# Performance work log

Measured on AMD Instinct MI355X. Metric: run time of the kernel, lower is better.

Reference implementation:

```python
import jax, jax.numpy as jnp
import numpy as np

N_NODES = 50000
N_EDGES = 800000
HID = 64
N_LAYERS = 4
POS_DIM = 3
PARAM_SCALE = 0.1
POS_HEAD_SCALE = 0.001  # xavier gain=0.001 on final pos Linear


def setup_inputs() -> dict:
    key = jax.random.key(0)
    ks = jax.random.split(key, 12)
    L, H = N_LAYERS, HID
    s = PARAM_SCALE
    return {
        "x": jax.random.normal(ks[0], (N_NODES, HID), jnp.float32),
        "pos": jax.random.normal(ks[1], (N_NODES, POS_DIM), jnp.float32),
        "edge_index": jax.random.randint(ks[2], (2, N_EDGES), 0, N_NODES, jnp.int32),
        # edge MLP: Linear(2H+1 -> H), SiLU, Linear(H -> H), SiLU
        "We1": jax.random.normal(ks[3], (L, 2 * H + 1, H), jnp.float32) * s,
        "be1": jnp.zeros((L, H), jnp.float32),
        "We2": jax.random.normal(ks[4], (L, H, H), jnp.float32) * s,
        "be2": jnp.zeros((L, H), jnp.float32),
        # node MLP: Linear(2H -> H), SiLU, Linear(H -> H)
        "Wn1": jax.random.normal(ks[5], (L, 2 * H, H), jnp.float32) * s,
        "bn1": jnp.zeros((L, H), jnp.float32),
        "Wn2": jax.random.normal(ks[6], (L, H, H), jnp.float32) * s,
        "bn2": jnp.zeros((L, H), jnp.float32),
        # pos MLP: Linear(H -> H), SiLU, Linear(H -> 1) (tiny init)
        "Wp1": jax.random.normal(ks[7], (L, H, H), jnp.float32) * s,
        "bp1": jnp.zeros((L, H), jnp.float32),
        "Wp2": jax.random.normal(ks[8], (L, H, 1), jnp.float32) * POS_HEAD_SCALE,
        "bp2": jnp.zeros((L, 1), jnp.float32),
        # logit(pos_scale=0.5) == 0
        "pos_scale_logit": jnp.zeros((1,), jnp.float32),
    }


def reference(x, pos, edge_index, We1, be1, We2, be2, Wn1, bn1, Wn2, bn2,
              Wp1, bp1, Wp2, bp2, pos_scale_logit):
    POS_CLAMP = 500.0
    POS_UPDATE_CLAMP = 5.0
    src, dst = edge_index[0], edge_index[1]  # messages flow j=src -> i=dst
    n = x.shape[0]
    L = We1.shape[0]

    # pos is NOT fed back between layers in the torch forward, so edge
    # geometry is constant across layers.
    rel = pos[dst] - pos[src]                     # [E, P]
    d2 = jnp.sum(rel * rel, axis=-1, keepdims=True)  # [E, 1]
    deg = jnp.maximum(
        jax.ops.segment_sum(jnp.ones(src.shape, x.dtype), dst, num_segments=n),
        1.0)[:, None]                             # [N, 1]

    pos_new = pos
    for l in range(L):
        # edge MLP on gathered node pairs
        m = jnp.concatenate([x[dst], x[src], d2], axis=-1)  # [E, 2H+1]
        m = jax.nn.silu(m @ We1[l] + be1[l])
        m = jax.nn.silu(m @ We2[l] + be2[l])                # [E, H]
        # scatter-aggregate messages to target nodes
        agg = jax.ops.segment_sum(m, dst, num_segments=n)   # [N, H]
        # node update MLP
        h = jax.nn.silu(jnp.concatenate([x, agg], axis=-1) @ Wn1[l] + bn1[l])
        x = h @ Wn2[l] + bn2[l]
        # position update: mean over incoming edges of rel * phi_pos(m)
        c = jax.nn.silu(m @ Wp1[l] + bp1[l]) @ Wp2[l] + bp2[l]  # [E, 1]
        pos_new = pos + jax.ops.segment_sum(rel * c, dst, num_segments=n) / deg

    upd = (pos_new - pos) * jax.nn.sigmoid(pos_scale_logit[0])
    upd = jnp.clip(upd, -POS_UPDATE_CLAMP, POS_UPDATE_CLAMP)
    pos_out = jnp.clip(pos + upd, -POS_CLAMP, POS_CLAMP)
    return x, pos_out
```

## Files before the change

kernel.cpp:

```cpp
#include <hip/hip_runtime.h>

#define NN 50000
#define NE 800000
#define NTILES 12500
#define TPB 10

typedef __attribute__((ext_vector_type(8))) short short8;
typedef __attribute__((ext_vector_type(4))) float f32x4;

__device__ __forceinline__ float silu_f(float v) {
    return v / (1.0f + __expf(-v));
}
__device__ __forceinline__ unsigned short f2bf(float f) {
    unsigned u = __float_as_uint(f);
    u += 0x7fffu + ((u >> 16) & 1u);
    return (unsigned short)(u >> 16);
}
__device__ __forceinline__ unsigned pk2(float a, float b) {
    return (unsigned)f2bf(a) | ((unsigned)f2bf(b) << 16);
}
__device__ __forceinline__ void gload_lds16(const unsigned short* g, unsigned short* l) {
    __builtin_amdgcn_global_load_lds(
        (const __attribute__((address_space(1))) unsigned int*)g,
        (__attribute__((address_space(3))) unsigned int*)l, 16, 0, 0);
}
#define FENCE_BAR() do { \
    asm volatile("s_waitcnt lgkmcnt(0)" ::: "memory"); \
    __builtin_amdgcn_sched_barrier(0); \
    __builtin_amdgcn_s_barrier(); \
    __builtin_amdgcn_sched_barrier(0); \
} while (0)
#define VMDRAIN() do { \
    __builtin_amdgcn_sched_barrier(0); \
    asm volatile("s_waitcnt vmcnt(0)" ::: "memory"); \
    __builtin_amdgcn_sched_barrier(0); \
} while (0)

__global__ __launch_bounds__(256) void egnn_hist(
    const int* __restrict__ dst, int* __restrict__ hc)
{
    int e = blockIdx.x * 256 + threadIdx.x;
    if (e < NE) atomicAdd(&hc[dst[e]], 1);
}

__global__ __launch_bounds__(1024) void egnn_scan(
    int* __restrict__ hc, int* __restrict__ rowptr)
{
    __shared__ int part[1024];
    const int t = threadIdx.x;
    const int C = (NN + 1023) / 1024;
    const int b0 = t * C;
    int s = 0;
    for (int i = 0; i < C; ++i) {
        int idx = b0 + i;
        if (idx < NN) s += hc[idx];
    }
    part[t] = s;
    __syncthreads();
    for (int off = 1; off < 1024; off <<= 1) {
        int v = (t >= off) ? part[t - off] : 0;
        __syncthreads();
        part[t] += v;
        __syncthreads();
    }
    int run = part[t] - s;
    for (int i = 0; i < C; ++i) {
        int idx = b0 + i;
        if (idx < NN) {
            int v = hc[idx];
            rowptr[idx] = run;
            hc[idx] = run;
            run += v;
        }
    }
    if (t == 1023) rowptr[NN] = part[1023];
}

__global__ __launch_bounds__(256) void egnn_scatter(
    const int* __restrict__ src, const int* __restrict__ dst,
    const float* __restrict__ pos, int* __restrict__ cursor,
    int* __restrict__ eSrc, int* __restrict__ eDst, float* __restrict__ eD2)
{
    int e = blockIdx.x * 256 + threadIdx.x;
    if (e >= NE) return;
    int s = src[e], d = dst[e];
    float rx = pos[3*d+0] - pos[3*s+0];
    float ry = pos[3*d+1] - pos[3*s+1];
    float rz = pos[3*d+2] - pos[3*s+2];
    int p = atomicAdd(&cursor[d], 1);
    eSrc[p] = s;
    eDst[p] = d;
    eD2[p]  = rx*rx + ry*ry + rz*rz;
}

__global__ __launch_bounds__(256) void egnn_prep_w(
    const float* __restrict__ We1, const float* __restrict__ We2,
    unsigned short* __restrict__ Wg1, unsigned short* __restrict__ Wg2)
{
    int i = blockIdx.x * 256 + threadIdx.x;
    if (i < 4 * 64 * 128) {
        int k = i & 127, n = (i >> 7) & 63, l = i >> 13;
        Wg1[(size_t)(l * 64 + n) * 136 + k] = f2bf(We1[((size_t)l * 129 + k) * 64 + n]);
    }
    if (i < 4 * 64 * 64) {
        int h = i & 63, n = (i >> 6) & 63, l = i >> 12;
        Wg2[(size_t)(l * 64 + n) * 72 + h] = f2bf(We2[((size_t)l * 64 + h) * 64 + n]);
    }
}

__global__ __launch_bounds__(256) void egnn_prep_wn(
    const float* __restrict__ Wn1, const float* __restrict__ Wn2,
    unsigned short* __restrict__ Wgn1, unsigned short* __restrict__ Wgn2)
{
    int i = blockIdx.x * 256 + threadIdx.x;
    if (i < 4 * 64 * 128) {
        int k = i & 127, n = (i >> 7) & 63, l = i >> 13;
        Wgn1[(size_t)(l * 64 + n) * 136 + k] = f2bf(Wn1[((size_t)l * 128 + k) * 64 + n]);
    }
    if (i < 4 * 64 * 64) {
        int h = i & 63, n = (i >> 6) & 63, l = i >> 12;
        Wgn2[(size_t)(l * 64 + n) * 72 + h] = f2bf(Wn2[((size_t)l * 64 + h) * 64 + n]);
    }
}

__global__ __launch_bounds__(256) void egnn_xbf(
    const float* __restrict__ x, unsigned short* __restrict__ xbf)
{
    int i = blockIdx.x * 256 + threadIdx.x;
    if (i >= NN * 16) return;
    float4 v = ((const float4*)x)[i];
    ((uint2*)xbf)[i] = make_uint2(pk2(v.x, v.y), pk2(v.z, v.w));
}

template<bool POS>
__global__ __launch_bounds__(256) void egnn_edge(
    const unsigned short* __restrict__ xbf, const float* __restrict__ eD2,
    const int* __restrict__ eSrc, const int* __restrict__ eDst,
    const float* __restrict__ pos,
    const unsigned short* __restrict__ Wg1, const unsigned short* __restrict__ Wg2,
    const float* __restrict__ We1,
    const float* __restrict__ be1, const float* __restrict__ be2,
    const float* __restrict__ Wp1, const float* __restrict__ bp1,
    const float* __restrict__ Wp2, const float* __restrict__ bp2,
    float* __restrict__ agg, float* __restrict__ dpos, int layer)
{
    __shared__ __align__(16) unsigned char pool[16384 * 2 + 16640];
    __shared__ int   sS[2][64];
    __shared__ int   sD[2][64];
    __shared__ float s2[2][64];
    __shared__ float sC[64];

    unsigned short* const xls0 = (unsigned short*)pool;
    unsigned short* const xls1 = (unsigned short*)(pool + 16384);
    unsigned short* const m1l  = (unsigned short*)(pool + 32768);
    float* const          sM2f = (float*)(pool + 32768);

    const int t    = threadIdx.x;
    const int lane = t & 63;
    const int w    = t >> 6;
    const int l15  = lane & 15;
    const int g    = lane >> 4;
    const int eh   = w >> 1;
    const int ch   = w & 1;
    const int er   = lane >> 4;
    const int half = (lane >> 3) & 1;
    const int c    = lane & 7;
    const int tile0 = blockIdx.x * TPB;

    const unsigned short* W1b = &Wg1[(size_t)(layer * 64) * 136];
    const unsigned short* W2b = &Wg2[(size_t)(layer * 64) * 72];
    short8 w1f0[4], w1f1[4], w2f0[2], w2f1[2];
    #pragma unroll
    for (int ks = 0; ks < 4; ++ks) {
        w1f0[ks] = *(const short8*)&W1b[(ch * 32 +      l15) * 136 + ks * 32 + g * 8];
        w1f1[ks] = *(const short8*)&W1b[(ch * 32 + 16 + l15) * 136 + ks * 32 + g * 8];
    }
    #pragma unroll
    for (int ks = 0; ks < 2; ++ks) {
        w2f0[ks] = *(const short8*)&W2b[(ch * 32 +      l15) * 72 + ks * 32 + g * 8];
        w2f1[ks] = *(const short8*)&W2b[(ch * 32 + 16 + l15) * 72 + ks * 32 + g * 8];
    }
    float4 wrv[2], b1v[2], b2v[2];
    {
        const float* Wr = &We1[((size_t)layer * 129 + 128) * 64];
        const float* B1 = &be1[layer * 64];
        const float* B2 = &be2[layer * 64];
        #pragma unroll
        for (int nt = 0; nt < 2; ++nt) {
            int n0 = ch * 32 + nt * 16 + g * 4;
            wrv[nt] = *(const float4*)&Wr[n0];
            b1v[nt] = *(const float4*)&B1[n0];
            b2v[nt] = *(const float4*)&B2[n0];
        }
    }

    const int* const ip = half ? eSrc : eDst;
    const int ebase = w * 16 + er;

    int nid[4];
    {
        const int gb0 = tile0 * 64;
        #pragma unroll
        for (int i = 0; i < 4; ++i) nid[i] = ip[gb0 + ebase + i * 4];
        #pragma unroll
        for (int i = 0; i < 4; ++i)
            gload_lds16(&xbf[(size_t)nid[i] * 64 + ((c ^ ((ebase + i * 4) & 7)) << 3)],
                        xls0 + w * 2048 + i * 512);
        __builtin_amdgcn_sched_barrier(0);
        #pragma unroll
        for (int i = 0; i < 4; ++i) nid[i] = ip[gb0 + 64 + ebase + i * 4];
        if (t < 64) { sS[0][t] = eSrc[gb0 + t]; sD[0][t] = eDst[gb0 + t]; s2[0][t] = eD2[gb0 + t]; }
    }
    int stS = 0, stD = 0; float st2 = 0.f;
    if (t < 64) {
        const int gb1 = (tile0 + 1) * 64;
        stS = eSrc[gb1 + t]; stD = eDst[gb1 + t]; st2 = eD2[gb1 + t];
    }
    float bp2v = 0.f;
    if (POS) { bp2v = bp2[layer]; if (t < 64) sC[t] = bp2v; }
    VMDRAIN();
    FENCE_BAR();

    const f32x4 zero = {0.f, 0.f, 0.f, 0.f};

    for (int tt = 0; tt < TPB; ++tt) {
        const int b = tt & 1;
        unsigned short* const xcur = b ? xls1 : xls0;
        unsigned short* const xnxt = b ? xls0 : xls1;

        if (tt + 1 < TPB) {
            #pragma unroll
            for (int i = 0; i < 4; ++i)
                gload_lds16(&xbf[(size_t)nid[i] * 64 + ((c ^ ((ebase + i * 4) & 7)) << 3)],
                            xnxt + w * 2048 + i * 512);
            __builtin_amdgcn_sched_barrier(0);
            if (tt + 2 < TPB) {
                const int gb2 = (tile0 + tt + 2) * 64;
                #pragma unroll
                for (int i = 0; i < 4; ++i) nid[i] = ip[gb2 + ebase + i * 4];
            }
        }

        f32x4 a00 = zero, a01 = zero, a10 = zero, a11 = zero;
        {
            const int r0 = (eh * 32 + l15) * 128;
            const int r1 = r0 + 16 * 128;
            const int r7 = l15 & 7;
            #pragma unroll
            for (int ks = 0; ks < 4; ++ks) {
                int col = (((ks << 2) + g) ^ r7) << 3;
                short8 fb0 = *(const short8*)&xcur[r0 + col];
                short8 fb1 = *(const short8*)&xcur[r1 + col];
                a00 = __builtin_amdgcn_mfma_f32_16x16x32_bf16(w1f0[ks], fb0, a00, 0, 0, 0);
                a01 = __builtin_amdgcn_mfma_f32_16x16x32_bf16(w1f0[ks], fb1, a01, 0, 0, 0);
                a10 = __builtin_amdgcn_mfma_f32_16x16x32_bf16(w1f1[ks], fb0, a10, 0, 0, 0);
                a11 = __builtin_amdgcn_mfma_f32_16x16x32_bf16(w1f1[ks], fb1, a11, 0, 0, 0);
            }
        }
        {
            float d2e0 = s2[b][eh * 32 + l15];
            float d2e1 = s2[b][eh * 32 + 16 + l15];
            int e0 = eh * 32 + l15;
            int e1 = e0 + 16;
            #pragma unroll
            for (int nt = 0; nt < 2; ++nt) {
                int n0 = ch * 32 + nt * 16 + g * 4;
                float4 wr = wrv[nt], bb = b1v[nt];
                f32x4 acc0 = nt ? a10 : a00;
                f32x4 acc1 = nt ? a11 : a01;
                float r0 = silu_f(acc0.x + d2e0 * wr.x + bb.x);
                float r1 = silu_f(acc0.y + d2e0 * wr.y + bb.y);
                float r2 = silu_f(acc0.z + d2e0 * wr.z + bb.z);
                float r3 = silu_f(acc0.w + d2e0 * wr.w + bb.w);
                *(uint2*)&m1l[e0 * 72 + n0] = make_uint2(pk2(r0, r1), pk2(r2, r3));
                r0 = silu_f(acc1.x + d2e1 * wr.x + bb.x);
                r1 = silu_f(acc1.y + d2e1 * wr.y + bb.y);
                r2 = silu_f(acc1.z + d2e1 * wr.z + bb.z);
                r3 = silu_f(acc1.w + d2e1 * wr.w + bb.w);
                *(uint2*)&m1l[e1 * 72 + n0] = make_uint2(pk2(r0, r1), pk2(r2, r3));
            }
        }
        FENCE_BAR();

        f32x4 c00 = zero, c01 = zero, c10 = zero, c11 = zero;
        #pragma unroll
        for (int ks = 0; ks < 2; ++ks) {
            short8 fb0 = *(const short8*)&m1l[(eh * 32 +      l15) * 72 + ks * 32 + g * 8];
            short8 fb1 = *(const short8*)&m1l[(eh * 32 + 16 + l15) * 72 + ks * 32 + g * 8];
            c00 = __builtin_amdgcn_mfma_f32_16x16x32_bf16(w2f0[ks], fb0, c00, 0, 0, 0);
            c01 = __builtin_amdgcn_mfma_f32_16x16x32_bf16(w2f0[ks], fb1, c01, 0, 0, 0);
            c10 = __builtin_amdgcn_mfma_f32_16x16x32_bf16(w2f1[ks], fb0, c10, 0, 0, 0);
            c11 = __builtin_amdgcn_mfma_f32_16x16x32_bf16(w2f1[ks], fb1, c11, 0, 0, 0);
        }
        FENCE_BAR();

        {
            int e0 = eh * 32 + l15;
            int e1 = e0 + 16;
            #pragma unroll
            for (int nt = 0; nt < 2; ++nt) {
                int n0 = ch * 32 + nt * 16 + g * 4;
                float4 bb = b2v[nt];
                f32x4 acc0 = nt ? c10 : c00;
                f32x4 acc1 = nt ? c11 : c01;
                sM2f[e0 * 65 + n0 + 0] = silu_f(acc0.x + bb.x);
                sM2f[e0 * 65 + n0 + 1] = silu_f(acc0.y + bb.y);
                sM2f[e0 * 65 + n0 + 2] = silu_f(acc0.z + bb.z);
                sM2f[e0 * 65 + n0 + 3] = silu_f(acc0.w + bb.w);
                sM2f[e1 * 65 + n0 + 0] = silu_f(acc1.x + bb.x);
                sM2f[e1 * 65 + n0 + 1] = silu_f(acc1.y + bb.y);
                sM2f[e1 * 65 + n0 + 2] = silu_f(acc1.z + bb.z);
                sM2f[e1 * 65 + n0 + 3] = silu_f(acc1.w + bb.w);
            }
        }
        if (tt + 1 < TPB && t < 64) {
            sS[1 - b][t] = stS; sD[1 - b][t] = stD; s2[1 - b][t] = st2;
            if (tt + 2 < TPB) {
                const int gb2 = (tile0 + tt + 2) * 64;
                stS = eSrc[gb2 + t]; stD = eDst[gb2 + t]; st2 = eD2[gb2 + t];
            }
        }
        FENCE_BAR();

        if (POS) {
            const int wofs = __builtin_amdgcn_readfirstlane(w * 16);
            float p1[16];
            {
                const float* bP1 = &bp1[(size_t)layer * 64 + wofs];
                #pragma unroll
                for (int hh = 0; hh < 16; ++hh) p1[hh] = bP1[hh];
            }
            const float* P1 = &Wp1[(size_t)layer * 64 * 64 + wofs];
            for (int k = 0; k < 64; ++k) {
                float mv = sM2f[lane * 65 + k];
                const float* wr2 = P1 + k * 64;
                #pragma unroll
                for (int hh = 0; hh < 16; ++hh) p1[hh] = fmaf(mv, wr2[hh], p1[hh]);
            }
            float part = 0.0f;
            {
                const float* P2 = &Wp2[(size_t)layer * 64 + wofs];
                #pragma unroll
                for (int hh = 0; hh < 16; ++hh) part += silu_f(p1[hh]) * P2[hh];
            }
            atomicAdd(&sC[lane], part);
            FENCE_BAR();
            if (w == 0) {
                float cc = sC[lane];
                int d = sD[b][lane], s = sS[b][lane];
                float rx = pos[3*d+0] - pos[3*s+0];
                float ry = pos[3*d+1] - pos[3*s+1];
                float rz = pos[3*d+2] - pos[3*s+2];
                atomicAdd(&dpos[3*(size_t)d+0], rx * cc);
                atomicAdd(&dpos[3*(size_t)d+1], ry * cc);
                atomicAdd(&dpos[3*(size_t)d+2], rz * cc);
            }
            FENCE_BAR();
            if (t < 64) sC[t] = bp2v;
        }

        VMDRAIN();

        {
            const int e0 = w * 16;
            float v[16];
            #pragma unroll
            for (int i = 0; i < 16; ++i) v[i] = sM2f[(e0 + i) * 65 + lane];
            int dd[16];
            #pragma unroll
            for (int i = 0; i < 16; ++i) dd[i] = sD[b][e0 + i];
            float run = v[0];
            int cur = dd[0];
            #pragma unroll
            for (int i = 1; i < 16; ++i) {
                if (dd[i] != cur) {
                    atomicAdd(&agg[(size_t)cur * 64 + lane], run);
                    run = 0.0f;
                    cur = dd[i];
                }
                run += v[i];
            }
            atomicAdd(&agg[(size_t)cur * 64 + lane], run);
        }
        FENCE_BAR();
    }
}

template<bool WRITE_F32>
__global__ __launch_bounds__(256) void egnn_node_mfma(
    const unsigned short* __restrict__ xbf, const float* __restrict__ agg,
    const unsigned short* __restrict__ Wgn1, const unsigned short* __restrict__ Wgn2,
    const float* __restrict__ bn1, const float* __restrict__ bn2,
    float* __restrict__ xout, unsigned short* __restrict__ xbf_out, int layer)
{
    __shared__ __align__(16) unsigned char pool[16384 + 9216];
    unsigned short* const xpl = (unsigned short*)pool;
    unsigned short* const m1l = (unsigned short*)(pool + 16384);
    float* const          sXf = (float*)pool;

    const int t    = threadIdx.x;
    const int lane = t & 63;
    const int w    = t >> 6;
    const int l15  = lane & 15;
    const int g    = lane >> 4;
    const int eh   = w >> 1;
    const int ch   = w & 1;
    const int base = blockIdx.x * 64;
    const int nval = (NN - base < 64) ? (NN - base) : 64;

    #pragma unroll
    for (int i = 0; i < 2; ++i) {
        int e = w * 16 + i * 8 + (lane >> 3);
        int node = base + ((e < nval) ? e : 0);
        gload_lds16(&xbf[(size_t)node * 64 + (((lane & 7) ^ (e & 7)) << 3)],
                    xpl + w * 1024 + i * 512);
    }
    __builtin_amdgcn_sched_barrier(0);

    const unsigned short* W1b = &Wgn1[(size_t)(layer * 64) * 136];
    const unsigned short* W2b = &Wgn2[(size_t)(layer * 64) * 72];
    short8 w1f0[4], w1f1[4], w2f0[2], w2f1[2];
    #pragma unroll
    for (int ks = 0; ks < 4; ++ks) {
        w1f0[ks] = *(const short8*)&W1b[(ch * 32 +      l15) * 136 + ks * 32 + g * 8];
        w1f1[ks] = *(const short8*)&W1b[(ch * 32 + 16 + l15) * 136 + ks * 32 + g * 8];
    }
    #pragma unroll
    for (int ks = 0; ks < 2; ++ks) {
        w2f0[ks] = *(const short8*)&W2b[(ch * 32 +      l15) * 72 + ks * 32 + g * 8];
        w2f1[ks] = *(const short8*)&W2b[(ch * 32 + 16 + l15) * 72 + ks * 32 + g * 8];
    }
    float4 b1v[2], b2v[2];
    {
        const float* B1 = &bn1[layer * 64];
        const float* B2 = &bn2[layer * 64];
        #pragma unroll
        for (int nt = 0; nt < 2; ++nt) {
            int n0 = ch * 32 + nt * 16 + g * 4;
            b1v[nt] = *(const float4*)&B1[n0];
            b2v[nt] = *(const float4*)&B2[n0];
        }
    }

    {
        int e = t >> 2, q = t & 3;
        int node = base + ((e < nval) ? e : 0);
        const float4* ap = (const float4*)&agg[(size_t)node * 64 + q * 16];
        float4 v0 = ap[0], v1 = ap[1], v2 = ap[2], v3 = ap[3];
        uint4 u0, u1;
        u0.x = pk2(v0.x, v0.y); u0.y = pk2(v0.z, v0.w);
        u0.z = pk2(v1.x, v1.y); u0.w = pk2(v1.z, v1.w);
        u1.x = pk2(v2.x, v2.y); u1.y = pk2(v2.z, v2.w);
        u1.z = pk2(v3.x, v3.y); u1.w = pk2(v3.z, v3.w);
        *(uint4*)&xpl[4096 + e * 64 + (((2 * q)     ^ (e & 7)) << 3)] = u0;
        *(uint4*)&xpl[4096 + e * 64 + (((2 * q + 1) ^ (e & 7)) << 3)] = u1;
    }
    __syncthreads();

    const f32x4 zero = {0.f, 0.f, 0.f, 0.f};
    f32x4 a00 = zero, a01 = zero, a10 = zero, a11 = zero;
    {
        const int e0 = eh * 32 + l15;
        const int e1 = e0 + 16;
        const int r7 = e0 & 7;
        #pragma unroll
        for (int ks = 0; ks < 4; ++ks) {
            int kc = (ks << 2) + g;
            int off0 = (kc >> 3) * 4096 + e0 * 64 + (((kc & 7) ^ r7) << 3);
            int off1 = (kc >> 3) * 4096 + e1 * 64 + (((kc & 7) ^ r7) << 3);
            short8 fb0 = *(const short8*)&xpl[off0];
            short8 fb1 = *(const short8*)&xpl[off1];
            a00 = __builtin_amdgcn_mfma_f32_16x16x32_bf16(w1f0[ks], fb0, a00, 0, 0, 0);
            a01 = __builtin_amdgcn_mfma_f32_16x16x32_bf16(w1f0[ks], fb1, a01, 0, 0, 0);
            a10 = __builtin_amdgcn_mfma_f32_16x16x32_bf16(w1f1[ks], fb0, a10, 0, 0, 0);
            a11 = __builtin_amdgcn_mfma_f32_16x16x32_bf16(w1f1[ks], fb1, a11, 0, 0, 0);
        }
    }
    {
        int e0 = eh * 32 + l15;
        int e1 = e0 + 16;
        #pragma unroll
        for (int nt = 0; nt < 2; ++nt) {
            int n0 = ch * 32 + nt * 16 + g * 4;
            float4 bb = b1v[nt];
            f32x4 acc0 = nt ? a10 : a00;
            f32x4 acc1 = nt ? a11 : a01;
            float r0 = silu_f(acc0.x + bb.x);
            float r1 = silu_f(acc0.y + bb.y);
            float r2 = silu_f(acc0.z + bb.z);
            float r3 = silu_f(acc0.w + bb.w);
            *(uint2*)&m1l[e0 * 72 + n0] = make_uint2(pk2(r0, r1), pk2(r2, r3));
            r0 = silu_f(acc1.x + bb.x);
            r1 = silu_f(acc1.y + bb.y);
            r2 = silu_f(acc1.z + bb.z);
            r3 = silu_f(acc1.w + bb.w);
            *(uint2*)&m1l[e1 * 72 + n0] = make_uint2(pk2(r0, r1), pk2(r2, r3));
        }
    }
    __syncthreads();

    f32x4 c00 = zero, c01 = zero, c10 = zero, c11 = zero;
    #pragma unroll
    for (int ks = 0; ks < 2; ++ks) {
        short8 fb0 = *(const short8*)&m1l[(eh * 32 +      l15) * 72 + ks * 32 + g * 8];
        short8 fb1 = *(const short8*)&m1l[(eh * 32 + 16 + l15) * 72 + ks * 32 + g * 8];
        c00 = __builtin_amdgcn_mfma_f32_16x16x32_bf16(w2f0[ks], fb0, c00, 0, 0, 0);
        c01 = __builtin_amdgcn_mfma_f32_16x16x32_bf16(w2f0[ks], fb1, c01, 0, 0, 0);
        c10 = __builtin_amdgcn_mfma_f32_16x16x32_bf16(w2f1[ks], fb0, c10, 0, 0, 0);
        c11 = __builtin_amdgcn_mfma_f32_16x16x32_bf16(w2f1[ks], fb1, c11, 0, 0, 0);
    }
    __syncthreads();

    {
        int e0 = eh * 32 + l15;
        int e1 = e0 + 16;
        #pragma unroll
        for (int nt = 0; nt < 2; ++nt) {
            int n0 = ch * 32 + nt * 16 + g * 4;
            float4 bb = b2v[nt];
            f32x4 acc0 = nt ? c10 : c00;
            f32x4 acc1 = nt ? c11 : c01;
            sXf[e0 * 65 + n0 + 0] = acc0.x + bb.x;
            sXf[e0 * 65 + n0 + 1] = acc0.y + bb.y;
            sXf[e0 * 65 + n0 + 2] = acc0.z + bb.z;
            sXf[e0 * 65 + n0 + 3] = acc0.w + bb.w;
            sXf[e1 * 65 + n0 + 0] = acc1.x + bb.x;
            sXf[e1 * 65 + n0 + 1] = acc1.y + bb.y;
            sXf[e1 * 65 + n0 + 2] = acc1.z + bb.z;
            sXf[e1 * 65 + n0 + 3] = acc1.w + bb.w;
        }
    }
    __syncthreads();

    if (WRITE_F32) {
        #pragma unroll
        for (int i = 0; i < 4; ++i) {
            int idx = i * 256 + t;
            int e = idx >> 4, c = idx & 15;
            if (e < nval) {
                float4 v;
                const float* p = &sXf[e * 65 + c * 4];
                v.x = p[0]; v.y = p[1]; v.z = p[2]; v.w = p[3];
                *reinterpret_cast<float4*>(&xout[(size_t)(base + e) * 64 + c * 4]) = v;
            }
        }
    }
    {
        int e = t >> 2, q = t & 3;
        if (e < nval) {
            const float* p = &sXf[e * 65 + q * 16];
            uint4 u0, u1;
            u0.x = pk2(p[0],  p[1]);  u0.y = pk2(p[2],  p[3]);
            u0.z = pk2(p[4],  p[5]);  u0.w = pk2(p[6],  p[7]);
            u1.x = pk2(p[8],  p[9]);  u1.y = pk2(p[10], p[11]);
            u1.z = pk2(p[12], p[13]); u1.w = pk2(p[14], p[15]);
            *(uint4*)&xbf_out[(size_t)(base + e) * 64 + q * 16 + 0] = u0;
            *(uint4*)&xbf_out[(size_t)(base + e) * 64 + q * 16 + 8] = u1;
        }
    }
}

__global__ __launch_bounds__(256) void egnn_final(
    const float* __restrict__ pos, const float* __restrict__ dpos,
    const int* __restrict__ rowptr, const float* __restrict__ logit,
    float* __restrict__ pos_out)
{
    int i = blockIdx.x * 256 + threadIdx.x;
    if (i >= NN * 3) return;
    int node = i / 3;
    float dg = fmaxf((float)(rowptr[node + 1] - rowptr[node]), 1.0f);
    float sig = 1.0f / (1.0f + __expf(-logit[0]));
    float upd = (dpos[i] / dg) * sig;
    upd = fminf(fmaxf(upd, -5.0f), 5.0f);
    float p = pos[i] + upd;
    pos_out[i] = fminf(fmaxf(p, -500.0f), 500.0f);
}

extern "C" void kernel_launch(void* const* d_in, const int* in_sizes, int n_in,
                              void* d_out, int out_size, void* d_ws, size_t ws_size,
                              hipStream_t stream)
{
    const float* x0    = (const float*)d_in[0];
    const float* pos   = (const float*)d_in[1];
    const int*   src   = (const int*)d_in[2];
    const int*   dst   = src + NE;
    const float* We1   = (const float*)d_in[3];
    const float* be1   = (const float*)d_in[4];
    const float* We2   = (const float*)d_in[5];
    const float* be2   = (const float*)d_in[6];
    const float* Wn1   = (const float*)d_in[7];
    const float* bn1   = (const float*)d_in[8];
    const float* Wn2   = (const float*)d_in[9];
    const float* bn2   = (const float*)d_in[10];
    const float* Wp1   = (const float*)d_in[11];
    const float* bp1   = (const float*)d_in[12];
    const float* Wp2   = (const float*)d_in[13];
    const float* bp2   = (const float*)d_in[14];
    const float* logit = (const float*)d_in[15];

    float* xout    = (float*)d_out;
    float* pos_out = xout + (size_t)NN * 64;

    float* ws  = (float*)d_ws;
    float* agg  = ws;  ws += (size_t)NN * 64;
    float* dpos = ws;  ws += (size_t)NN * 3;
    float* eD2  = ws;  ws += NE;
    int* rowptr = (int*)ws;  ws += NN + 1;
    int* hc     = (int*)ws;  ws += NN;
    int* eSrc   = (int*)ws;  ws += NE;
    int* eDst   = (int*)ws;  ws += NE;
    unsigned short* xbf = (unsigned short*)ws;
    ws += (size_t)NN * 32;
    unsigned short* Wg1  = (unsigned short*)ws;
    unsigned short* Wg2  = Wg1 + 4 * 64 * 136;
    unsigned short* Wgn1 = Wg2 + 4 * 64 * 72;
    unsigned short* Wgn2 = Wgn1 + 4 * 64 * 136;

    hipMemsetAsync(hc, 0, NN * sizeof(int), stream);
    hipMemsetAsync(dpos, 0, (size_t)NN * 3 * sizeof(float), stream);
    egnn_hist<<<NE / 256, 256, 0, stream>>>(dst, hc);
    egnn_scan<<<1, 1024, 0, stream>>>(hc, rowptr);
    egnn_scatter<<<NE / 256, 256, 0, stream>>>(src, dst, pos, hc, eSrc, eDst, eD2);
    egnn_prep_w<<<128, 256, 0, stream>>>(We1, We2, Wg1, Wg2);
    egnn_prep_wn<<<128, 256, 0, stream>>>(Wn1, Wn2, Wgn1, Wgn2);
    egnn_xbf<<<(NN * 16 + 255) / 256, 256, 0, stream>>>(x0, xbf);

    const int nblk = NTILES / TPB;
    const int nodeblk = (NN + 63) / 64;
    for (int l = 0; l < 4; ++l) {
        hipMemsetAsync(agg, 0, (size_t)NN * 64 * sizeof(float), stream);
        if (l == 3) {
            egnn_edge<true><<<nblk, 256, 0, stream>>>(
                xbf, eD2, eSrc, eDst, pos, Wg1, Wg2, We1, be1, be2,
                Wp1, bp1, Wp2, bp2, agg, dpos, l);
            egnn_node_mfma<true><<<nodeblk, 256, 0, stream>>>(
                xbf, agg, Wgn1, Wgn2, bn1, bn2, xout, xbf, l);
        } else {
            egnn_edge<false><<<nblk, 256, 0, stream>>>(
                xbf, eD2, eSrc, eDst, pos, Wg1, Wg2, We1, be1, be2,
                Wp1, bp1, Wp2, bp2, agg, dpos, l);
            egnn_node_mfma<false><<<nodeblk, 256, 0, stream>>>(
                xbf, agg, Wgn1, Wgn2, bn1, bn2, xout, xbf, l);
        }
    }
    egnn_final<<<(NN * 3 + 255) / 256, 256, 0, stream>>>(pos, dpos, rowptr, logit, pos_out);
}
```

Baseline: 901.5 us.

## Compute position MLP with bf16 MFMA and store edge messages as bf16

The last-layer position MLP (Wp1 matvec, SiLU, Wp2 dot) moves from scalar FMAs over fp32 LDS to bf16 MFMA, with Wp1 pre-transposed to bf16 in the prep kernel. The per-edge reduction now uses wave shuffles instead of shared atomics and extra barriers. Edge messages m2 are kept in LDS as bf16 instead of fp32, which cuts LDS footprint and removes one barrier. The cost is lower precision in the aggregated messages and in the position coefficients.

New measurement: 853.9 us. 5.3% less time.

```diff
diff --git a/kernel.cpp b/kernel.cpp
--- a/kernel.cpp
+++ b/kernel.cpp
@@ -18,6 +18,9 @@
 }
 __device__ __forceinline__ unsigned pk2(float a, float b) {
     return (unsigned)f2bf(a) | ((unsigned)f2bf(b) << 16);
+}
+__device__ __forceinline__ float bf2f(unsigned short v) {
+    return __uint_as_float((unsigned)v << 16);
 }
 __device__ __forceinline__ void gload_lds16(const unsigned short* g, unsigned short* l) {
     __builtin_amdgcn_global_load_lds(
@@ -95,7 +98,9 @@
 
 __global__ __launch_bounds__(256) void egnn_prep_w(
     const float* __restrict__ We1, const float* __restrict__ We2,
-    unsigned short* __restrict__ Wg1, unsigned short* __restrict__ Wg2)
+    const float* __restrict__ Wp1,
+    unsigned short* __restrict__ Wg1, unsigned short* __restrict__ Wg2,
+    unsigned short* __restrict__ Wgp1)
 {
     int i = blockIdx.x * 256 + threadIdx.x;
     if (i < 4 * 64 * 128) {
@@ -104,7 +109,8 @@
     }
     if (i < 4 * 64 * 64) {
         int h = i & 63, n = (i >> 6) & 63, l = i >> 12;
-        Wg2[(size_t)(l * 64 + n) * 72 + h] = f2bf(We2[((size_t)l * 64 + h) * 64 + n]);
+        Wg2[(size_t)(l * 64 + n) * 72 + h]  = f2bf(We2[((size_t)l * 64 + h) * 64 + n]);
+        Wgp1[(size_t)(l * 64 + n) * 72 + h] = f2bf(Wp1[((size_t)l * 64 + h) * 64 + n]);
     }
 }
 
@@ -138,28 +144,29 @@
     const int* __restrict__ eSrc, const int* __restrict__ eDst,
     const float* __restrict__ pos,
     const unsigned short* __restrict__ Wg1, const unsigned short* __restrict__ Wg2,
+    const unsigned short* __restrict__ Wgp1,
     const float* __restrict__ We1,
     const float* __restrict__ be1, const float* __restrict__ be2,
-    const float* __restrict__ Wp1, const float* __restrict__ bp1,
-    const float* __restrict__ Wp2, const float* __restrict__ bp2,
+    const float* __restrict__ bp1, const float* __restrict__ Wp2,
+    const float* __restrict__ bp2,
     float* __restrict__ agg, float* __restrict__ dpos, int layer)
 {
-    __shared__ __align__(16) unsigned char pool[16384 * 2 + 16640];
+    __shared__ __align__(16) unsigned char pool[16384 * 2 + 9216 * 2];
     __shared__ int   sS[2][64];
     __shared__ int   sD[2][64];
     __shared__ float s2[2][64];
-    __shared__ float sC[64];
 
     unsigned short* const xls0 = (unsigned short*)pool;
     unsigned short* const xls1 = (unsigned short*)(pool + 16384);
     unsigned short* const m1l  = (unsigned short*)(pool + 32768);
-    float* const          sM2f = (float*)(pool + 32768);
+    unsigned short* const m2s  = (unsigned short*)(pool + 41984);
 
     const int t    = threadIdx.x;
     const int lane = t & 63;
     const int w    = t >> 6;
     const int l15  = lane & 15;
     const int g    = lane >> 4;
+    const int g4   = g * 4;
     const int eh   = w >> 1;
     const int ch   = w & 1;
     const int er   = lane >> 4;
@@ -193,6 +200,16 @@
             b2v[nt] = *(const float4*)&B2[n0];
         }
     }
+    float4 b1p[4], w2p[4];
+    float bp2v = 0.f;
+    if (POS) {
+        #pragma unroll
+        for (int m = 0; m < 4; ++m) {
+            b1p[m] = *(const float4*)&bp1[(size_t)layer * 64 + m * 16 + g4];
+            w2p[m] = *(const float4*)&Wp2[(size_t)layer * 64 + m * 16 + g4];
+        }
+        bp2v = bp2[layer];
+    }
 
     const int* const ip = half ? eSrc : eDst;
     const int ebase = w * 16 + er;
@@ -216,8 +233,6 @@
         const int gb1 = (tile0 + 1) * 64;
         stS = eSrc[gb1 + t]; stD = eDst[gb1 + t]; st2 = eD2[gb1 + t];
     }
-    float bp2v = 0.f;
-    if (POS) { bp2v = bp2[layer]; if (t < 64) sC[t] = bp2v; }
     VMDRAIN();
     FENCE_BAR();
 
@@ -292,7 +307,6 @@
             c10 = __builtin_amdgcn_mfma_f32_16x16x32_bf16(w2f1[ks], fb0, c10, 0, 0, 0);
             c11 = __builtin_amdgcn_mfma_f32_16x16x32_bf16(w2f1[ks], fb1, c11, 0, 0, 0);
         }
-        FENCE_BAR();
 
         {
             int e0 = eh * 32 + l15;
@@ -303,14 +317,16 @@
                 float4 bb = b2v[nt];
                 f32x4 acc0 = nt ? c10 : c00;
                 f32x4 acc1 = nt ? c11 : c01;
-                sM2f[e0 * 65 + n0 + 0] = silu_f(acc0.x + bb.x);
-                sM2f[e0 * 65 + n0 + 1] = silu_f(acc0.y + bb.y);
-                sM2f[e0 * 65 + n0 + 2] = silu_f(acc0.z + bb.z);
-                sM2f[e0 * 65 + n0 + 3] = silu_f(acc0.w + bb.w);
-                sM2f[e1 * 65 + n0 + 0] = silu_f(acc1.x + bb.x);
-                sM2f[e1 * 65 + n0 + 1] = silu_f(acc1.y + bb.y);
-                sM2f[e1 * 65 + n0 + 2] = silu_f(acc1.z + bb.z);
-                sM2f[e1 * 65 + n0 + 3] = silu_f(acc1.w + bb.w);
+                float r0 = silu_f(acc0.x + bb.x);
+                float r1 = silu_f(acc0.y + bb.y);
+                float r2 = silu_f(acc0.z + bb.z);
+                float r3 = silu_f(acc0.w + bb.w);
+                *(uint2*)&m2s[e0 * 72 + n0] = make_uint2(pk2(r0, r1), pk2(r2, r3));
+                r0 = silu_f(acc1.x + bb.x);
+                r1 = silu_f(acc1.y + bb.y);
+                r2 = silu_f(acc1.z + bb.z);
+                r3 = silu_f(acc1.w + bb.w);
+                *(uint2*)&m2s[e1 * 72 + n0] = make_uint2(pk2(r0, r1), pk2(r2, r3));
             }
         }
         if (tt + 1 < TPB && t < 64) {
@@ -323,40 +339,38 @@
         FENCE_BAR();
 
         if (POS) {
-            const int wofs = __builtin_amdgcn_readfirstlane(w * 16);
-            float p1[16];
-            {
-                const float* bP1 = &bp1[(size_t)layer * 64 + wofs];
+            f32x4 pa[4] = {zero, zero, zero, zero};
+            const unsigned short* WPb = &Wgp1[(size_t)(layer * 64) * 72];
+            #pragma unroll
+            for (int ks = 0; ks < 2; ++ks) {
+                short8 fb = *(const short8*)&m2s[(w * 16 + l15) * 72 + ks * 32 + g * 8];
                 #pragma unroll
-                for (int hh = 0; hh < 16; ++hh) p1[hh] = bP1[hh];
-            }
-            const float* P1 = &Wp1[(size_t)layer * 64 * 64 + wofs];
-            for (int k = 0; k < 64; ++k) {
-                float mv = sM2f[lane * 65 + k];
-                const float* wr2 = P1 + k * 64;
-                #pragma unroll
-                for (int hh = 0; hh < 16; ++hh) p1[hh] = fmaf(mv, wr2[hh], p1[hh]);
+                for (int m = 0; m < 4; ++m) {
+                    short8 wf = *(const short8*)&WPb[(size_t)(m * 16 + l15) * 72 + ks * 32 + g * 8];
+                    pa[m] = __builtin_amdgcn_mfma_f32_16x16x32_bf16(wf, fb, pa[m], 0, 0, 0);
+                }
             }
             float part = 0.0f;
-            {
-                const float* P2 = &Wp2[(size_t)layer * 64 + wofs];
-                #pragma unroll
-                for (int hh = 0; hh < 16; ++hh) part += silu_f(p1[hh]) * P2[hh];
-            }
-            atomicAdd(&sC[lane], part);
-            FENCE_BAR();
-            if (w == 0) {
-                float cc = sC[lane];
-                int d = sD[b][lane], s = sS[b][lane];
+            #pragma unroll
+            for (int m = 0; m < 4; ++m) {
+                part += silu_f(pa[m].x + b1p[m].x) * w2p[m].x;
+                part += silu_f(pa[m].y + b1p[m].y) * w2p[m].y;
+                part += silu_f(pa[m].z + b1p[m].z) * w2p[m].z;
+                part += silu_f(pa[m].w + b1p[m].w) * w2p[m].w;
+            }
+            part += __shfl_xor(part, 16);
+            part += __shfl_xor(part, 32);
+            if (lane < 16) {
+                float cv = part + bp2v;
+                int idx16 = w * 16 + lane;
+                int d = sD[b][idx16], s = sS[b][idx16];
                 float rx = pos[3*d+0] - pos[3*s+0];
                 float ry = pos[3*d+1] - pos[3*s+1];
                 float rz = pos[3*d+2] - pos[3*s+2];
-                atomicAdd(&dpos[3*(size_t)d+0], rx * cc);
-                atomicAdd(&dpos[3*(size_t)d+1], ry * cc);
-                atomicAdd(&dpos[3*(size_t)d+2], rz * cc);
-            }
-            FENCE_BAR();
-            if (t < 64) sC[t] = bp2v;
+                atomicAdd(&dpos[3*(size_t)d+0], rx * cv);
+                atomicAdd(&dpos[3*(size_t)d+1], ry * cv);
+                atomicAdd(&dpos[3*(size_t)d+2], rz * cv);
+            }
         }
 
         VMDRAIN();
@@ -365,7 +379,7 @@
             const int e0 = w * 16;
             float v[16];
             #pragma unroll
-            for (int i = 0; i < 16; ++i) v[i] = sM2f[(e0 + i) * 65 + lane];
+            for (int i = 0; i < 16; ++i) v[i] = bf2f(m2s[(e0 + i) * 72 + lane]);
             int dd[16];
             #pragma unroll
             for (int i = 0; i < 16; ++i) dd[i] = sD[b][e0 + i];
@@ -615,13 +629,14 @@
     unsigned short* Wg2  = Wg1 + 4 * 64 * 136;
     unsigned short* Wgn1 = Wg2 + 4 * 64 * 72;
     unsigned short* Wgn2 = Wgn1 + 4 * 64 * 136;
+    unsigned short* Wgp1 = Wgn2 + 4 * 64 * 72;
 
     hipMemsetAsync(hc, 0, NN * sizeof(int), stream);
     hipMemsetAsync(dpos, 0, (size_t)NN * 3 * sizeof(float), stream);
     egnn_hist<<<NE / 256, 256, 0, stream>>>(dst, hc);
     egnn_scan<<<1, 1024, 0, stream>>>(hc, rowptr);
     egnn_scatter<<<NE / 256, 256, 0, stream>>>(src, dst, pos, hc, eSrc, eDst, eD2);
-    egnn_prep_w<<<128, 256, 0, stream>>>(We1, We2, Wg1, Wg2);
+    egnn_prep_w<<<128, 256, 0, stream>>>(We1, We2, Wp1, Wg1, Wg2, Wgp1);
     egnn_prep_wn<<<128, 256, 0, stream>>>(Wn1, Wn2, Wgn1, Wgn2);
     egnn_xbf<<<(NN * 16 + 255) / 256, 256, 0, stream>>>(x0, xbf);
 
@@ -631,14 +646,14 @@
         hipMemsetAsync(agg, 0, (size_t)NN * 64 * sizeof(float), stream);
         if (l == 3) {
             egnn_edge<true><<<nblk, 256, 0, stream>>>(
-                xbf, eD2, eSrc, eDst, pos, Wg1, Wg2, We1, be1, be2,
-                Wp1, bp1, Wp2, bp2, agg, dpos, l);
+                xbf, eD2, eSrc, eDst, pos, Wg1, Wg2, Wgp1, We1, be1, be2,
+                bp1, Wp2, bp2, agg, dpos, l);
             egnn_node_mfma<true><<<nodeblk, 256, 0, stream>>>(
                 xbf, agg, Wgn1, Wgn2, bn1, bn2, xout, xbf, l);
         } else {
             egnn_edge<false><<<nblk, 256, 0, stream>>>(
-                xbf, eD2, eSrc, eDst, pos, Wg1, Wg2, We1, be1, be2,
-                Wp1, bp1, Wp2, bp2, agg, dpos, l);
+                xbf, eD2, eSrc, eDst, pos, Wg1, Wg2, Wgp1, We1, be1, be2,
+                bp1, Wp2, bp2, agg, dpos, l);
             egnn_node_mfma<false><<<nodeblk, 256, 0, stream>>>(
                 xbf, agg, Wgn1, Wgn2, bn1, bn2, xout, xbf, l);
         }
```
